# Performance work log

Hardware: AMD Instinct MI355X
Metric: run time of the kernel (lower is better)

Reference implementation:

```python
import jax, jax.numpy as jnp
import numpy as np

N, E = 50000, 800000
NFEAT, HID, NHEAD, NCLASS = 256, 32, 8, 40
NEG_SLOPE = 0.2


def gat_conv(x, src, dst, W, a_src, a_dst, bias, heads, out_ch, concat):
    n = x.shape[0]
    h = (x @ W).reshape(n, heads, out_ch)              # [N, H, C]
    alpha_src = jnp.einsum('nhc,hc->nh', h, a_src)     # [N, H]
    alpha_dst = jnp.einsum('nhc,hc->nh', h, a_dst)
    e = jax.nn.leaky_relu(alpha_src[src] + alpha_dst[dst], NEG_SLOPE)  # [E, H]
    # segment softmax over incoming edges of each dst node
    m = jax.ops.segment_max(e, dst, num_segments=n)
    ex = jnp.exp(e - m[dst])
    s = jax.ops.segment_sum(ex, dst, num_segments=n)
    alpha = ex / (s[dst] + 1e-16)                      # [E, H]
    out = jax.ops.segment_sum(h[src] * alpha[:, :, None], dst, num_segments=n)  # [N, H, C]
    out = out.reshape(n, heads * out_ch) if concat else out.mean(axis=1)
    return out + bias


def setup_inputs() -> dict:
    key = jax.random.key(0)
    ks = jax.random.split(key, 12)
    x = jax.random.normal(ks[0], (N, NFEAT), dtype=jnp.float32)
    edge_index = jax.random.randint(ks[1], (2, E), 0, N, dtype=jnp.int64)
    edge_attr = jax.random.normal(ks[2], (E, 8), dtype=jnp.float32)  # unused by the model
    s1 = 1.0 / np.sqrt(NFEAT)
    s2 = 1.0 / np.sqrt(HID * NHEAD)
    W1 = jax.random.normal(ks[3], (NFEAT, NHEAD * HID), dtype=jnp.float32) * s1
    att_src1 = jax.random.normal(ks[4], (NHEAD, HID), dtype=jnp.float32) * 0.1
    att_dst1 = jax.random.normal(ks[5], (NHEAD, HID), dtype=jnp.float32) * 0.1
    b1 = jnp.zeros((NHEAD * HID,), dtype=jnp.float32)
    W2 = jax.random.normal(ks[6], (NHEAD * HID, NCLASS), dtype=jnp.float32) * s2
    att_src2 = jax.random.normal(ks[7], (1, NCLASS), dtype=jnp.float32) * 0.1
    att_dst2 = jax.random.normal(ks[8], (1, NCLASS), dtype=jnp.float32) * 0.1
    b2 = jnp.zeros((NCLASS,), dtype=jnp.float32)
    return {"x": x, "edge_index": edge_index, "edge_attr": edge_attr,
            "W1": W1, "att_src1": att_src1, "att_dst1": att_dst1, "b1": b1,
            "W2": W2, "att_src2": att_src2, "att_dst2": att_dst2, "b2": b2}


def reference(x, edge_index, edge_attr, W1, att_src1, att_dst1, b1, W2, att_src2, att_dst2, b2):
    # eval mode: dropout is identity. GATConv adds self-loops by default.
    n = x.shape[0]
    loops = jnp.arange(n, dtype=edge_index.dtype)
    src = jnp.concatenate([edge_index[0], loops])
    dst = jnp.concatenate([edge_index[1], loops])
    h = jax.nn.elu(gat_conv(x, src, dst, W1, att_src1, att_dst1, b1, NHEAD, HID, True))
    final = gat_conv(h, src, dst, W2, att_src2, att_dst2, b2, 1, NCLASS, False)
    return final, jax.nn.log_softmax(final, axis=1)
```

## Files before the change

kernel.cpp:

```cpp
#include <hip/hip_runtime.h>
#include <hip/hip_bf16.h>
#include <hip/hip_fp16.h>
#include <math.h>

#define NN 50000
#define EE 800000
#define ET 850000
#define F1 256
#define NHEAD 8
#define HID 32
#define NCLASS 40
#define NEG 0.2f

typedef __attribute__((ext_vector_type(8))) short short8_t;
typedef __attribute__((ext_vector_type(4))) float float4_t;

__device__ __forceinline__ int clampN(int v) {
    return v < 0 ? 0 : (v >= NN ? NN - 1 : v);
}
__device__ __forceinline__ unsigned short f2bf(float f) {
    __hip_bfloat16 h = __float2bfloat16(f);
    return __builtin_bit_cast(unsigned short, h);
}
__device__ __forceinline__ float bf2f(unsigned short u) {
    return __uint_as_float((unsigned)u << 16);
}
__device__ __forceinline__ unsigned short f2h(float f) {
    __half h = __float2half(f);
    return __builtin_bit_cast(unsigned short, h);
}
__device__ __forceinline__ float h2f(unsigned short u) {
    __half h = __builtin_bit_cast(__half, u);
    return __half2float(h);
}
__device__ __forceinline__ float hlo2f(unsigned int u) {
    return h2f((unsigned short)(u & 0xFFFFu));
}
__device__ __forceinline__ float hhi2f(unsigned int u) {
    return h2f((unsigned short)(u >> 16));
}

__global__ __launch_bounds__(256) void hist_kernel(const int* __restrict__ ei, int* __restrict__ deg,
                                                   unsigned int* __restrict__ pack) {
    int t = blockIdx.x * 256 + threadIdx.x;
    if (t >= ET) return;
    int d = (t < EE) ? ei[EE + t] : (t - EE);
    d = clampN(d);
    int r = atomicAdd(&deg[d], 1);
    pack[t] = ((unsigned)d << 15) | (unsigned)r;
}

__global__ __launch_bounds__(256) void scan1_kernel(const int* __restrict__ deg, int* __restrict__ off, int* __restrict__ bsum) {
    __shared__ int lds[256];
    int b = blockIdx.x, tid = threadIdx.x;
    int base = b * 1024 + tid * 4;
    int v0 = (base + 0 < NN) ? deg[base + 0] : 0;
    int v1 = (base + 1 < NN) ? deg[base + 1] : 0;
    int v2 = (base + 2 < NN) ? deg[base + 2] : 0;
    int v3 = (base + 3 < NN) ? deg[base + 3] : 0;
    int s1 = v0 + v1, s2 = s1 + v2, s3 = s2 + v3;
    lds[tid] = s3;
    __syncthreads();
    for (int o = 1; o < 256; o <<= 1) {
        int t = (tid >= o) ? lds[tid - o] : 0;
        __syncthreads();
        if (tid >= o) lds[tid] += t;
        __syncthreads();
    }
    int excl = tid ? lds[tid - 1] : 0;
    if (base + 0 < NN) off[base + 1] = excl + v0;
    if (base + 1 < NN) off[base + 2] = excl + s1;
    if (base + 2 < NN) off[base + 3] = excl + s2;
    if (base + 3 < NN) off[base + 4] = excl + s3;
    if (tid == 255) bsum[b] = lds[255];
}

__global__ __launch_bounds__(256) void scan2_kernel(int* __restrict__ bsum, int nb) {
    __shared__ int lds[256];
    int tid = threadIdx.x;
    lds[tid] = (tid < nb) ? bsum[tid] : 0;
    __syncthreads();
    for (int o = 1; o < 256; o <<= 1) {
        int t = (tid >= o) ? lds[tid - o] : 0;
        __syncthreads();
        if (tid >= o) lds[tid] += t;
        __syncthreads();
    }
    if (tid < nb) bsum[tid] = lds[tid];
}

__global__ __launch_bounds__(256) void scan3_kernel(int* __restrict__ off, const int* __restrict__ bsum) {
    int b = blockIdx.x, tid = threadIdx.x;
    if (b == 0 && tid == 0) off[0] = 0;
    if (b == 0) return;
    int add = bsum[b - 1];
    int base = b * 1024 + tid * 4;
    #pragma unroll
    for (int i = 0; i < 4; ++i) {
        if (base + i < NN) off[base + i + 1] += add;
    }
}

__global__ __launch_bounds__(256) void scatter_kernel(const int* __restrict__ ei, const int* __restrict__ off,
                                                      const unsigned int* __restrict__ pack, int* __restrict__ esrc) {
    int t = blockIdx.x * 256 + threadIdx.x;
    if (t >= ET) return;
    unsigned p = pack[t];
    int d = p >> 15;
    int r = p & 0x7FFF;
    int s = (t < EE) ? ei[t] : (t - EE);
    s = clampN(s);
    esrc[off[d] + r] = s;
}

__global__ __launch_bounds__(256) void prep_kernel(const float* __restrict__ W1,
                                                   const float* __restrict__ as1, const float* __restrict__ ad1,
                                                   unsigned short* __restrict__ Bh, unsigned short* __restrict__ Bl) {
    int n = blockIdx.x;
    int k = threadIdx.x;
    float v;
    if (n < 256) {
        v = W1[(size_t)k * 256 + n];
    } else {
        int j = n - 256;
        int h = j & 7;
        const float* att = (j < 8) ? (as1 + h * 32) : (ad1 + h * 32);
        float s = 0.f;
        #pragma unroll
        for (int c = 0; c < 32; ++c) s += W1[(size_t)k * 256 + h * 32 + c] * att[c];
        v = s;
    }
    unsigned short hi = f2bf(v);
    Bh[n * 256 + k] = hi;
    Bl[n * 256 + k] = f2bf(v - bf2f(hi));
}

#define AKP 40
__global__ __launch_bounds__(256, 2) void gemm1_kernel(const float* __restrict__ x,
                                                       const unsigned short* __restrict__ Bh,
                                                       const unsigned short* __restrict__ Bl,
                                                       unsigned short* __restrict__ h1b,
                                                       float* __restrict__ asrc1, float* __restrict__ adst1) {
    __shared__ __align__(16) unsigned short Ah[128 * AKP];
    __shared__ __align__(16) unsigned short Al[128 * AKP];
    __shared__ __align__(16) unsigned short Bhs[272 * AKP];
    __shared__ __align__(16) unsigned short Bls[272 * AKP];
    int tid = threadIdx.x;
    int wave = tid >> 6, lane = tid & 63;
    int quad = lane >> 4, l16 = lane & 15;
    int row0 = blockIdx.x * 128;

    float4_t acc[2][17];
    #pragma unroll
    for (int i = 0; i < 2; ++i)
        #pragma unroll
        for (int j = 0; j < 17; ++j) acc[i][j] = (float4_t){0.f, 0.f, 0.f, 0.f};

    for (int k0 = 0; k0 < 256; k0 += 32) {
        __syncthreads();
        #pragma unroll
        for (int i = 0; i < 4; ++i) {
            int id = i * 256 + tid;
            int r = id >> 3, kq = id & 7;
            int rr = row0 + r; if (rr >= NN) rr = NN - 1;
            float4 v = *(const float4*)(x + (size_t)rr * 256 + k0 + kq * 4);
            ushort4 hi, lo;
            hi.x = f2bf(v.x); lo.x = f2bf(v.x - bf2f(hi.x));
            hi.y = f2bf(v.y); lo.y = f2bf(v.y - bf2f(hi.y));
            hi.z = f2bf(v.z); lo.z = f2bf(v.z - bf2f(hi.z));
            hi.w = f2bf(v.w); lo.w = f2bf(v.w - bf2f(hi.w));
            *(ushort4*)(Ah + r * AKP + kq * 4) = hi;
            *(ushort4*)(Al + r * AKP + kq * 4) = lo;
        }
        for (int id = tid; id < 272 * 4; id += 256) {
            int r = id >> 2, kq = id & 3;
            *(float4*)(Bhs + r * AKP + kq * 8) = *(const float4*)(Bh + (size_t)r * 256 + k0 + kq * 8);
            *(float4*)(Bls + r * AKP + kq * 8) = *(const float4*)(Bl + (size_t)r * 256 + k0 + kq * 8);
        }
        __syncthreads();
        short8_t ah[2], al[2];
        #pragma unroll
        for (int mt = 0; mt < 2; ++mt) {
            int mrow = wave * 32 + mt * 16 + l16;
            ah[mt] = *(const short8_t*)(Ah + mrow * AKP + quad * 8);
            al[mt] = *(const short8_t*)(Al + mrow * AKP + quad * 8);
        }
        #pragma unroll
        for (int nt = 0; nt < 17; ++nt) {
            int nrow = nt * 16 + l16;
            short8_t bh  = *(const short8_t*)(Bhs + nrow * AKP + quad * 8);
            short8_t blo = *(const short8_t*)(Bls + nrow * AKP + quad * 8);
            #pragma unroll
            for (int mt = 0; mt < 2; ++mt) {
                acc[mt][nt] = __builtin_amdgcn_mfma_f32_16x16x32_bf16(ah[mt], bh,  acc[mt][nt], 0, 0, 0);
                acc[mt][nt] = __builtin_amdgcn_mfma_f32_16x16x32_bf16(ah[mt], blo, acc[mt][nt], 0, 0, 0);
                acc[mt][nt] = __builtin_amdgcn_mfma_f32_16x16x32_bf16(al[mt], bh,  acc[mt][nt], 0, 0, 0);
            }
        }
    }
    #pragma unroll
    for (int mt = 0; mt < 2; ++mt) {
        int rbase = row0 + wave * 32 + mt * 16 + quad * 4;
        #pragma unroll
        for (int r = 0; r < 4; ++r) {
            int row = rbase + r;
            if (row >= NN) continue;
            #pragma unroll
            for (int nt = 0; nt < 16; ++nt)
                h1b[(size_t)row * 256 + nt * 16 + l16] = f2h(acc[mt][nt][r]);
            float v = acc[mt][16][r];
            if (l16 < 8) asrc1[row * 8 + l16] = v;
            else         adst1[row * 8 + (l16 - 8)] = v;
        }
    }
}

#define WST 68
__global__ __launch_bounds__(256) void agg1_kernel(const unsigned short* __restrict__ h1b, const float* __restrict__ asrc,
                                                   const float* __restrict__ adst, const int* __restrict__ esrc,
                                                   const int* __restrict__ off,
                                                   const float* __restrict__ b1, unsigned short* __restrict__ hout) {
    __shared__ __align__(16) float wl[4][8 * WST];
    __shared__ __align__(16) int  snl[4][64];
    int tid = threadIdx.x;
    int wave = tid >> 6;
    int wid = blockIdx.x * 4 + wave;
    if (wid >= NN) return;
    int lane = tid & 63;
    int hp = lane & 7;
    int jp = lane >> 3;
    int hc = lane >> 3;
    int c0 = lane * 4;
    float adh_p = adst[wid * 8 + hp];
    int e0 = off[wid], e1 = off[wid + 1];
    float* wlw = wl[wave];
    int* snw = snl[wave];
    const char* hb = (const char*)h1b;
    unsigned lofs = (unsigned)c0 * 2;

    float m = -INFINITY, s = 0.f;
    float ax = 0.f, ay = 0.f, az = 0.f, aw = 0.f;

    for (int base = e0; base < e1; base += 64) {
        int cnt = e1 - base; if (cnt > 64) cnt = 64;
        int snv = esrc[base + (lane < cnt ? lane : cnt - 1)];
        snw[lane] = snv;
        int nch = (cnt + 7) >> 3;
        float ee[8];
        float wmax = -INFINITY;
        #pragma unroll
        for (int cj = 0; cj < 8; ++cj) {
            if (cj >= nch) { ee[cj] = -INFINITY; continue; }
            int jedge = cj * 8 + jp;
            int sj = __shfl(snv, jedge);
            float a = asrc[sj * 8 + hp];
            float e = a + adh_p;
            e = (e >= 0.f) ? e : NEG * e;
            if (jedge >= cnt) e = -INFINITY;
            ee[cj] = e;
            wmax = fmaxf(wmax, e);
        }
        wmax = fmaxf(wmax, __shfl_xor(wmax, 8));
        wmax = fmaxf(wmax, __shfl_xor(wmax, 16));
        wmax = fmaxf(wmax, __shfl_xor(wmax, 32));
        float mn = fmaxf(m, wmax);
        float t = __expf(m - mn);
        m = mn;
        s *= t;
        float tc = __shfl(t, hc);
        ax *= tc; ay *= tc; az *= tc; aw *= tc;
        #pragma unroll
        for (int cj = 0; cj < 8; ++cj) {
            if (cj >= nch) break;
            float w = __expf(ee[cj] - mn);
            s += w;
            wlw[hp * WST + cj * 8 + jp] = w;
        }
        const float* wrow = wlw + hc * WST;
        for (int j = 0; j < cnt; j += 4) {
            float4 w4 = *(const float4*)(wrow + j);
            int4 sn4 = *(const int4*)(snw + j);
            uint2 u0 = *(const uint2*)(hb + (((unsigned)sn4.x << 9) + lofs));
            uint2 u1 = *(const uint2*)(hb + (((unsigned)sn4.y << 9) + lofs));
            uint2 u2 = *(const uint2*)(hb + (((unsigned)sn4.z << 9) + lofs));
            uint2 u3 = *(const uint2*)(hb + (((unsigned)sn4.w << 9) + lofs));
            ax += w4.x * hlo2f(u0.x);
            ay += w4.x * hhi2f(u0.x);
            az += w4.x * hlo2f(u0.y);
            aw += w4.x * hhi2f(u0.y);
            ax += w4.y * hlo2f(u1.x);
            ay += w4.y * hhi2f(u1.x);
            az += w4.y * hlo2f(u1.y);
            aw += w4.y * hhi2f(u1.y);
            ax += w4.z * hlo2f(u2.x);
            ay += w4.z * hhi2f(u2.x);
            az += w4.z * hlo2f(u2.y);
            aw += w4.z * hhi2f(u2.y);
            ax += w4.w * hlo2f(u3.x);
            ay += w4.w * hhi2f(u3.x);
            az += w4.w * hlo2f(u3.y);
            aw += w4.w * hhi2f(u3.y);
        }
    }
    s += __shfl_xor(s, 8);
    s += __shfl_xor(s, 16);
    s += __shfl_xor(s, 32);
    float sh = __shfl(s, hc);
    float inv = 1.f / (sh + 1e-16f);
    float4 b = *(const float4*)(b1 + c0);
    float vx = ax * inv + b.x, vy = ay * inv + b.y, vz = az * inv + b.z, vw = aw * inv + b.w;
    ushort4 o;
    o.x = f2h((vx > 0.f) ? vx : expm1f(vx));
    o.y = f2h((vy > 0.f) ? vy : expm1f(vy));
    o.z = f2h((vz > 0.f) ? vz : expm1f(vz));
    o.w = f2h((vw > 0.f) ? vw : expm1f(vw));
    *(ushort4*)(hout + (size_t)wid * 256 + c0) = o;
}

#define G2_TM 128
#define G2_KC 32
__global__ __launch_bounds__(256) void gemm2_kernel(const unsigned short* __restrict__ h, const float* __restrict__ W2,
                                                    const float* __restrict__ at_s, const float* __restrict__ at_d,
                                                    unsigned short* __restrict__ h2b, float* __restrict__ as2,
                                                    float* __restrict__ ad2) {
    __shared__ __align__(16) float w2s[256 * 40];
    __shared__ __align__(16) float As[G2_KC][132];
    int tid = threadIdx.x;
    for (int i = tid; i < 256 * 40; i += 256) w2s[i] = W2[i];
    int g  = tid & 7;
    int rg = tid >> 3;
    int row0 = blockIdx.x * G2_TM;
    float acc[4][5] = {};
    float ats[5], atd[5];
    #pragma unroll
    for (int j = 0; j < 5; ++j) { ats[j] = at_s[g + 8 * j]; atd[j] = at_d[g + 8 * j]; }

    for (int k0 = 0; k0 < 256; k0 += G2_KC) {
        __syncthreads();
        #pragma unroll
        for (int i = 0; i < 2; ++i) {
            int id = i * 256 + tid;
            int r  = id >> 2;
            int kq = id & 3;
            int rr = row0 + r; if (rr >= NN) rr = NN - 1;
            uint4 u = *(const uint4*)(h + (size_t)rr * 256 + k0 + kq * 8);
            As[kq * 8 + 0][r] = hlo2f(u.x);
            As[kq * 8 + 1][r] = hhi2f(u.x);
            As[kq * 8 + 2][r] = hlo2f(u.y);
            As[kq * 8 + 3][r] = hhi2f(u.y);
            As[kq * 8 + 4][r] = hlo2f(u.z);
            As[kq * 8 + 5][r] = hhi2f(u.z);
            As[kq * 8 + 6][r] = hlo2f(u.w);
            As[kq * 8 + 7][r] = hhi2f(u.w);
        }
        __syncthreads();
        #pragma unroll 4
        for (int k = 0; k < G2_KC; ++k) {
            float4 a = *(const float4*)(&As[k][rg * 4]);
            float w[5];
            #pragma unroll
            for (int j = 0; j < 5; ++j) w[j] = w2s[(k0 + k) * 40 + g + 8 * j];
            float av[4] = {a.x, a.y, a.z, a.w};
            #pragma unroll
            for (int r = 0; r < 4; ++r)
                #pragma unroll
                for (int j = 0; j < 5; ++j)
                    acc[r][j] += av[r] * w[j];
        }
    }

    #pragma unroll
    for (int r = 0; r < 4; ++r) {
        int row = row0 + rg * 4 + r;
        float ps = 0.f, pd = 0.f;
        #pragma unroll
        for (int j = 0; j < 5; ++j) {
            ps += acc[r][j] * ats[j];
            pd += acc[r][j] * atd[j];
        }
        ps += __shfl_xor(ps, 1); pd += __shfl_xor(pd, 1);
        ps += __shfl_xor(ps, 2); pd += __shfl_xor(pd, 2);
        ps += __shfl_xor(ps, 4); pd += __shfl_xor(pd, 4);
        if (row < NN) {
            #pragma unroll
            for (int j = 0; j < 5; ++j) h2b[(size_t)row * 40 + g + 8 * j] = f2h(acc[r][j]);
            if (g == 0) { as2[row] = ps; ad2[row] = pd; }
        }
    }
}

__global__ __launch_bounds__(256) void agg2_kernel(const unsigned short* __restrict__ h2b, const float* __restrict__ asrc,
                                                   const float* __restrict__ adst, const int* __restrict__ esrc,
                                                   const int* __restrict__ off,
                                                   const float* __restrict__ b2, float* __restrict__ outF,
                                                   float* __restrict__ outL) {
    __shared__ __align__(16) float wl2[4][64];
    __shared__ __align__(16) int  snl2[4][64];
    int tid = threadIdx.x;
    int wave = tid >> 6;
    int wid = blockIdx.x * 4 + wave;
    if (wid >= NN) return;
    int lane = tid & 63;
    int c = lane;
    float adh = adst[wid];
    int e0 = off[wid], e1 = off[wid + 1];
    const char* hb = (const char*)h2b + ((unsigned)(c < NCLASS ? c : 0) << 1);
    float* wlw = wl2[wave];
    int* snw = snl2[wave];

    float m = -INFINITY, s = 0.f, acc = 0.f;

    for (int base = e0; base < e1; base += 64) {
        int cnt = e1 - base; if (cnt > 64) cnt = 64;
        int snv = esrc[base + (lane < cnt ? lane : cnt - 1)];
        snw[lane] = snv;
        float a = asrc[snv];
        float e = a + adh;
        e = (e >= 0.f) ? e : NEG * e;
        if (lane >= cnt) e = -INFINITY;
        float cm = e;
        cm = fmaxf(cm, __shfl_xor(cm, 1));
        cm = fmaxf(cm, __shfl_xor(cm, 2));
        cm = fmaxf(cm, __shfl_xor(cm, 4));
        cm = fmaxf(cm, __shfl_xor(cm, 8));
        cm = fmaxf(cm, __shfl_xor(cm, 16));
        cm = fmaxf(cm, __shfl_xor(cm, 32));
        float mn = fmaxf(m, cm);
        float t = __expf(m - mn);
        float w = __expf(e - mn);
        s = s * t + w;
        m = mn;
        wlw[lane] = w;
        acc *= t;
        for (int j = 0; j < cnt; j += 4) {
            float4 w4 = *(const float4*)(wlw + j);
            int4 sn4 = *(const int4*)(snw + j);
            unsigned short v0 = *(const unsigned short*)(hb + (unsigned)sn4.x * 80);
            unsigned short v1 = *(const unsigned short*)(hb + (unsigned)sn4.y * 80);
            unsigned short v2 = *(const unsigned short*)(hb + (unsigned)sn4.z * 80);
            unsigned short v3 = *(const unsigned short*)(hb + (unsigned)sn4.w * 80);
            acc += w4.x * h2f(v0);
            acc += w4.y * h2f(v1);
            acc += w4.z * h2f(v2);
            acc += w4.w * h2f(v3);
        }
    }
    s += __shfl_xor(s, 1);
    s += __shfl_xor(s, 2);
    s += __shfl_xor(s, 4);
    s += __shfl_xor(s, 8);
    s += __shfl_xor(s, 16);
    s += __shfl_xor(s, 32);
    float inv = 1.f / (s + 1e-16f);
    float fin = (c < NCLASS) ? (acc * inv + b2[c]) : -INFINITY;
    if (c < NCLASS) outF[(size_t)wid * 40 + c] = fin;
    float mx = fin;
    for (int o = 32; o; o >>= 1) mx = fmaxf(mx, __shfl_xor(mx, o));
    float ex = (c < NCLASS) ? __expf(fin - mx) : 0.f;
    float sm = ex;
    for (int o = 32; o; o >>= 1) sm += __shfl_xor(sm, o);
    if (c < NCLASS) outL[(size_t)wid * 40 + c] = fin - mx - __logf(sm);
}

extern "C" void kernel_launch(void* const* d_in, const int* in_sizes, int n_in,
                              void* d_out, int out_size, void* d_ws, size_t ws_size,
                              hipStream_t stream) {
    const float* x   = (const float*)d_in[0];
    const int*   ei  = (const int*)d_in[1];
    const float* W1  = (const float*)d_in[3];
    const float* as1 = (const float*)d_in[4];
    const float* ad1 = (const float*)d_in[5];
    const float* b1  = (const float*)d_in[6];
    const float* W2  = (const float*)d_in[7];
    const float* as2c = (const float*)d_in[8];
    const float* ad2c = (const float*)d_in[9];
    const float* b2  = (const float*)d_in[10];

    float* outF = (float*)d_out;
    float* outL = outF + (size_t)NN * NCLASS;

    char* w = (char*)d_ws;
    auto alloc = [&](size_t bytes) {
        void* p = (void*)w;
        w += (bytes + 255) & ~(size_t)255;
        return p;
    };
    unsigned short* h1b = (unsigned short*)alloc((size_t)NN * 256 * 2);
    unsigned short* hbuf = (unsigned short*)alloc((size_t)NN * 256 * 2);
    unsigned short* h2b = (unsigned short*)alloc((size_t)NN * 40 * 2);
    float* asrc1 = (float*)alloc((size_t)NN * 8 * 4);
    float* adst1 = (float*)alloc((size_t)NN * 8 * 4);
    float* asrc2 = (float*)alloc((size_t)NN * 4);
    float* adst2 = (float*)alloc((size_t)NN * 4);
    int* deg    = (int*)alloc((size_t)NN * 4);
    int* off    = (int*)alloc((size_t)(NN + 1) * 4);
    unsigned int* pack = (unsigned int*)alloc((size_t)ET * 4);
    int* esrc   = (int*)alloc((size_t)ET * 4);
    int* bsum   = (int*)alloc(64 * 4);
    unsigned short* W1th = (unsigned short*)alloc((size_t)272 * 256 * 2);
    unsigned short* W1tl = (unsigned short*)alloc((size_t)272 * 256 * 2);

    const int NB_SCAN = (NN + 1023) / 1024;

    hipMemsetAsync(deg, 0, (size_t)NN * 4, stream);

    hist_kernel<<<(ET + 255) / 256, 256, 0, stream>>>(ei, deg, pack);
    scan1_kernel<<<NB_SCAN, 256, 0, stream>>>(deg, off, bsum);
    scan2_kernel<<<1, 256, 0, stream>>>(bsum, NB_SCAN);
    scan3_kernel<<<NB_SCAN, 256, 0, stream>>>(off, bsum);
    scatter_kernel<<<(ET + 255) / 256, 256, 0, stream>>>(ei, off, pack, esrc);

    prep_kernel<<<272, 256, 0, stream>>>(W1, as1, ad1, W1th, W1tl);
    gemm1_kernel<<<(NN + 127) / 128, 256, 0, stream>>>(x, W1th, W1tl, h1b, asrc1, adst1);
    agg1_kernel<<<(NN + 3) / 4, 256, 0, stream>>>(h1b, asrc1, adst1, esrc, off, b1, hbuf);
    gemm2_kernel<<<(NN + G2_TM - 1) / G2_TM, 256, 0, stream>>>(hbuf, W2, as2c, ad2c, h2b, asrc2, adst2);
    agg2_kernel<<<(NN + 3) / 4, 256, 0, stream>>>(h2b, asrc2, adst2, esrc, off, b2, outF, outL);
}
```

Measured before the change: 341.3 us.

## Use fp16 split GEMM and process two destination nodes per wave in aggregation

The first GEMM now splits only x into hi/lo fp16 parts and keeps W1 as a single fp16 matrix, so each tile issues two MFMAs instead of three and stages half the B data. Both aggregation kernels now handle two destination nodes per wave, interleaving their gather loads with scalar (readfirstlane) row addresses and unrolling by 8 edges. This is meant to raise memory-level parallelism and hide gather latency. The trade-offs are lower precision on W1, extra register pressure, and wasted work when the two nodes have very different degrees.

```diff
diff --git a/kernel.cpp b/kernel.cpp
--- a/kernel.cpp
+++ b/kernel.cpp
@@ -13,17 +13,11 @@
 #define NEG 0.2f
 
 typedef __attribute__((ext_vector_type(8))) short short8_t;
+typedef __attribute__((ext_vector_type(8))) _Float16 half8_t;
 typedef __attribute__((ext_vector_type(4))) float float4_t;
 
 __device__ __forceinline__ int clampN(int v) {
     return v < 0 ? 0 : (v >= NN ? NN - 1 : v);
-}
-__device__ __forceinline__ unsigned short f2bf(float f) {
-    __hip_bfloat16 h = __float2bfloat16(f);
-    return __builtin_bit_cast(unsigned short, h);
-}
-__device__ __forceinline__ float bf2f(unsigned short u) {
-    return __uint_as_float((unsigned)u << 16);
 }
 __device__ __forceinline__ unsigned short f2h(float f) {
     __half h = __float2half(f);
@@ -115,7 +109,7 @@
 
 __global__ __launch_bounds__(256) void prep_kernel(const float* __restrict__ W1,
                                                    const float* __restrict__ as1, const float* __restrict__ ad1,
-                                                   unsigned short* __restrict__ Bh, unsigned short* __restrict__ Bl) {
+                                                   unsigned short* __restrict__ Bt) {
     int n = blockIdx.x;
     int k = threadIdx.x;
     float v;
@@ -130,21 +124,17 @@
         for (int c = 0; c < 32; ++c) s += W1[(size_t)k * 256 + h * 32 + c] * att[c];
         v = s;
     }
-    unsigned short hi = f2bf(v);
-    Bh[n * 256 + k] = hi;
-    Bl[n * 256 + k] = f2bf(v - bf2f(hi));
+    Bt[n * 256 + k] = f2h(v);
 }
 
 #define AKP 40
 __global__ __launch_bounds__(256, 2) void gemm1_kernel(const float* __restrict__ x,
-                                                       const unsigned short* __restrict__ Bh,
-                                                       const unsigned short* __restrict__ Bl,
+                                                       const unsigned short* __restrict__ Bt,
                                                        unsigned short* __restrict__ h1b,
                                                        float* __restrict__ asrc1, float* __restrict__ adst1) {
     __shared__ __align__(16) unsigned short Ah[128 * AKP];
     __shared__ __align__(16) unsigned short Al[128 * AKP];
-    __shared__ __align__(16) unsigned short Bhs[272 * AKP];
-    __shared__ __align__(16) unsigned short Bls[272 * AKP];
+    __shared__ __align__(16) unsigned short Bs[272 * AKP];
     int tid = threadIdx.x;
     int wave = tid >> 6, lane = tid & 63;
     int quad = lane >> 4, l16 = lane & 15;
@@ -165,36 +155,33 @@
             int rr = row0 + r; if (rr >= NN) rr = NN - 1;
             float4 v = *(const float4*)(x + (size_t)rr * 256 + k0 + kq * 4);
             ushort4 hi, lo;
-            hi.x = f2bf(v.x); lo.x = f2bf(v.x - bf2f(hi.x));
-            hi.y = f2bf(v.y); lo.y = f2bf(v.y - bf2f(hi.y));
-            hi.z = f2bf(v.z); lo.z = f2bf(v.z - bf2f(hi.z));
-            hi.w = f2bf(v.w); lo.w = f2bf(v.w - bf2f(hi.w));
+            hi.x = f2h(v.x); lo.x = f2h(v.x - h2f(hi.x));
+            hi.y = f2h(v.y); lo.y = f2h(v.y - h2f(hi.y));
+            hi.z = f2h(v.z); lo.z = f2h(v.z - h2f(hi.z));
+            hi.w = f2h(v.w); lo.w = f2h(v.w - h2f(hi.w));
             *(ushort4*)(Ah + r * AKP + kq * 4) = hi;
             *(ushort4*)(Al + r * AKP + kq * 4) = lo;
         }
         for (int id = tid; id < 272 * 4; id += 256) {
             int r = id >> 2, kq = id & 3;
-            *(float4*)(Bhs + r * AKP + kq * 8) = *(const float4*)(Bh + (size_t)r * 256 + k0 + kq * 8);
-            *(float4*)(Bls + r * AKP + kq * 8) = *(const float4*)(Bl + (size_t)r * 256 + k0 + kq * 8);
+            *(float4*)(Bs + r * AKP + kq * 8) = *(const float4*)(Bt + (size_t)r * 256 + k0 + kq * 8);
         }
         __syncthreads();
-        short8_t ah[2], al[2];
+        half8_t ah[2], al[2];
         #pragma unroll
         for (int mt = 0; mt < 2; ++mt) {
             int mrow = wave * 32 + mt * 16 + l16;
-            ah[mt] = *(const short8_t*)(Ah + mrow * AKP + quad * 8);
-            al[mt] = *(const short8_t*)(Al + mrow * AKP + quad * 8);
+            ah[mt] = *(const half8_t*)(Ah + mrow * AKP + quad * 8);
+            al[mt] = *(const half8_t*)(Al + mrow * AKP + quad * 8);
         }
         #pragma unroll
         for (int nt = 0; nt < 17; ++nt) {
             int nrow = nt * 16 + l16;
-            short8_t bh  = *(const short8_t*)(Bhs + nrow * AKP + quad * 8);
-            short8_t blo = *(const short8_t*)(Bls + nrow * AKP + quad * 8);
+            half8_t bh = *(const half8_t*)(Bs + nrow * AKP + quad * 8);
             #pragma unroll
             for (int mt = 0; mt < 2; ++mt) {
-                acc[mt][nt] = __builtin_amdgcn_mfma_f32_16x16x32_bf16(ah[mt], bh,  acc[mt][nt], 0, 0, 0);
-                acc[mt][nt] = __builtin_amdgcn_mfma_f32_16x16x32_bf16(ah[mt], blo, acc[mt][nt], 0, 0, 0);
-                acc[mt][nt] = __builtin_amdgcn_mfma_f32_16x16x32_bf16(al[mt], bh,  acc[mt][nt], 0, 0, 0);
+                acc[mt][nt] = __builtin_amdgcn_mfma_f32_16x16x32_f16(ah[mt], bh, acc[mt][nt], 0, 0, 0);
+                acc[mt][nt] = __builtin_amdgcn_mfma_f32_16x16x32_f16(al[mt], bh, acc[mt][nt], 0, 0, 0);
             }
         }
     }
@@ -220,101 +207,219 @@
                                                    const float* __restrict__ adst, const int* __restrict__ esrc,
                                                    const int* __restrict__ off,
                                                    const float* __restrict__ b1, unsigned short* __restrict__ hout) {
-    __shared__ __align__(16) float wl[4][8 * WST];
-    __shared__ __align__(16) int  snl[4][64];
+    __shared__ __align__(16) float wl[4][2][8 * WST];
+    __shared__ __align__(16) int  snl[4][2][64];
     int tid = threadIdx.x;
     int wave = tid >> 6;
-    int wid = blockIdx.x * 4 + wave;
-    if (wid >= NN) return;
+    int wid0 = blockIdx.x * 8 + wave * 2;
+    if (wid0 >= NN) return;
+    int wid1 = wid0 + 1;
+    bool has1 = (wid1 < NN);
     int lane = tid & 63;
     int hp = lane & 7;
     int jp = lane >> 3;
     int hc = lane >> 3;
     int c0 = lane * 4;
-    float adh_p = adst[wid * 8 + hp];
-    int e0 = off[wid], e1 = off[wid + 1];
-    float* wlw = wl[wave];
-    int* snw = snl[wave];
+    float* wlw0 = wl[wave][0];
+    float* wlw1 = wl[wave][1];
+    int* snw0 = snl[wave][0];
+    int* snw1 = snl[wave][1];
+    const float* wrow0 = wlw0 + hc * WST;
+    const float* wrow1 = wlw1 + hc * WST;
     const char* hb = (const char*)h1b;
     unsigned lofs = (unsigned)c0 * 2;
-
-    float m = -INFINITY, s = 0.f;
-    float ax = 0.f, ay = 0.f, az = 0.f, aw = 0.f;
-
-    for (int base = e0; base < e1; base += 64) {
-        int cnt = e1 - base; if (cnt > 64) cnt = 64;
-        int snv = esrc[base + (lane < cnt ? lane : cnt - 1)];
-        snw[lane] = snv;
-        int nch = (cnt + 7) >> 3;
-        float ee[8];
-        float wmax = -INFINITY;
-        #pragma unroll
-        for (int cj = 0; cj < 8; ++cj) {
-            if (cj >= nch) { ee[cj] = -INFINITY; continue; }
-            int jedge = cj * 8 + jp;
-            int sj = __shfl(snv, jedge);
-            float a = asrc[sj * 8 + hp];
-            float e = a + adh_p;
-            e = (e >= 0.f) ? e : NEG * e;
-            if (jedge >= cnt) e = -INFINITY;
-            ee[cj] = e;
-            wmax = fmaxf(wmax, e);
-        }
-        wmax = fmaxf(wmax, __shfl_xor(wmax, 8));
-        wmax = fmaxf(wmax, __shfl_xor(wmax, 16));
-        wmax = fmaxf(wmax, __shfl_xor(wmax, 32));
-        float mn = fmaxf(m, wmax);
-        float t = __expf(m - mn);
-        m = mn;
-        s *= t;
-        float tc = __shfl(t, hc);
-        ax *= tc; ay *= tc; az *= tc; aw *= tc;
-        #pragma unroll
-        for (int cj = 0; cj < 8; ++cj) {
-            if (cj >= nch) break;
-            float w = __expf(ee[cj] - mn);
-            s += w;
-            wlw[hp * WST + cj * 8 + jp] = w;
-        }
-        const float* wrow = wlw + hc * WST;
-        for (int j = 0; j < cnt; j += 4) {
-            float4 w4 = *(const float4*)(wrow + j);
-            int4 sn4 = *(const int4*)(snw + j);
-            uint2 u0 = *(const uint2*)(hb + (((unsigned)sn4.x << 9) + lofs));
-            uint2 u1 = *(const uint2*)(hb + (((unsigned)sn4.y << 9) + lofs));
-            uint2 u2 = *(const uint2*)(hb + (((unsigned)sn4.z << 9) + lofs));
-            uint2 u3 = *(const uint2*)(hb + (((unsigned)sn4.w << 9) + lofs));
-            ax += w4.x * hlo2f(u0.x);
-            ay += w4.x * hhi2f(u0.x);
-            az += w4.x * hlo2f(u0.y);
-            aw += w4.x * hhi2f(u0.y);
-            ax += w4.y * hlo2f(u1.x);
-            ay += w4.y * hhi2f(u1.x);
-            az += w4.y * hlo2f(u1.y);
-            aw += w4.y * hhi2f(u1.y);
-            ax += w4.z * hlo2f(u2.x);
-            ay += w4.z * hhi2f(u2.x);
-            az += w4.z * hlo2f(u2.y);
-            aw += w4.z * hhi2f(u2.y);
-            ax += w4.w * hlo2f(u3.x);
-            ay += w4.w * hhi2f(u3.x);
-            az += w4.w * hlo2f(u3.y);
-            aw += w4.w * hhi2f(u3.y);
-        }
-    }
-    s += __shfl_xor(s, 8);
-    s += __shfl_xor(s, 16);
-    s += __shfl_xor(s, 32);
-    float sh = __shfl(s, hc);
-    float inv = 1.f / (sh + 1e-16f);
+    float adh0 = adst[wid0 * 8 + hp];
+    float adh1 = has1 ? adst[wid1 * 8 + hp] : 0.f;
+    int e1_0 = off[wid0 + 1], base0 = off[wid0];
+    int e1_1 = has1 ? off[wid1 + 1] : 0;
+    int base1 = has1 ? off[wid1] : 0;
+
+    float m0 = -INFINITY, s0 = 0.f;
+    float m1 = -INFINITY, s1 = 0.f;
+    float ax0 = 0.f, ay0 = 0.f, az0 = 0.f, aw0 = 0.f;
+    float ax1 = 0.f, ay1 = 0.f, az1 = 0.f, aw1 = 0.f;
+
+    while (base0 < e1_0 || base1 < e1_1) {
+        int cnt0 = e1_0 - base0; cnt0 = cnt0 < 0 ? 0 : (cnt0 > 64 ? 64 : cnt0);
+        int cnt1 = e1_1 - base1; cnt1 = cnt1 < 0 ? 0 : (cnt1 > 64 ? 64 : cnt1);
+        int nch0 = (cnt0 + 7) >> 3;
+        int nch1 = (cnt1 + 7) >> 3;
+        int snv0 = 0, snv1 = 0;
+        if (cnt0 > 0) { snv0 = esrc[base0 + (lane < cnt0 ? lane : cnt0 - 1)]; snw0[lane] = snv0; }
+        if (cnt1 > 0) { snv1 = esrc[base1 + (lane < cnt1 ? lane : cnt1 - 1)]; snw1[lane] = snv1; }
+        float ee0[8], ee1[8];
+        float wmax0 = -INFINITY, wmax1 = -INFINITY;
+        if (cnt0 > 0) {
+            #pragma unroll
+            for (int cj = 0; cj < 8; ++cj) {
+                if (cj >= nch0) { ee0[cj] = -INFINITY; continue; }
+                int jedge = cj * 8 + jp;
+                int sj = __shfl(snv0, jedge);
+                float a = asrc[sj * 8 + hp];
+                float e = a + adh0;
+                e = (e >= 0.f) ? e : NEG * e;
+                if (jedge >= cnt0) e = -INFINITY;
+                ee0[cj] = e;
+                wmax0 = fmaxf(wmax0, e);
+            }
+        }
+        if (cnt1 > 0) {
+            #pragma unroll
+            for (int cj = 0; cj < 8; ++cj) {
+                if (cj >= nch1) { ee1[cj] = -INFINITY; continue; }
+                int jedge = cj * 8 + jp;
+                int sj = __shfl(snv1, jedge);
+                float a = asrc[sj * 8 + hp];
+                float e = a + adh1;
+                e = (e >= 0.f) ? e : NEG * e;
+                if (jedge >= cnt1) e = -INFINITY;
+                ee1[cj] = e;
+                wmax1 = fmaxf(wmax1, e);
+            }
+        }
+        if (cnt0 > 0) {
+            wmax0 = fmaxf(wmax0, __shfl_xor(wmax0, 8));
+            wmax0 = fmaxf(wmax0, __shfl_xor(wmax0, 16));
+            wmax0 = fmaxf(wmax0, __shfl_xor(wmax0, 32));
+            float mn = fmaxf(m0, wmax0);
+            float t = __expf(m0 - mn);
+            m0 = mn;
+            s0 *= t;
+            float tc = __shfl(t, hc);
+            ax0 *= tc; ay0 *= tc; az0 *= tc; aw0 *= tc;
+            #pragma unroll
+            for (int cj = 0; cj < 8; ++cj) {
+                if (cj >= nch0) break;
+                float w = __expf(ee0[cj] - mn);
+                s0 += w;
+                wlw0[hp * WST + cj * 8 + jp] = w;
+            }
+        }
+        if (cnt1 > 0) {
+            wmax1 = fmaxf(wmax1, __shfl_xor(wmax1, 8));
+            wmax1 = fmaxf(wmax1, __shfl_xor(wmax1, 16));
+            wmax1 = fmaxf(wmax1, __shfl_xor(wmax1, 32));
+            float mn = fmaxf(m1, wmax1);
+            float t = __expf(m1 - mn);
+            m1 = mn;
+            s1 *= t;
+            float tc = __shfl(t, hc);
+            ax1 *= tc; ay1 *= tc; az1 *= tc; aw1 *= tc;
+            #pragma unroll
+            for (int cj = 0; cj < 8; ++cj) {
+                if (cj >= nch1) break;
+                float w = __expf(ee1[cj] - mn);
+                s1 += w;
+                wlw1[hp * WST + cj * 8 + jp] = w;
+            }
+        }
+        int nslots0 = (cnt0 > 0) ? nch0 * 8 : 0;
+        int nslots1 = (cnt1 > 0) ? nch1 * 8 : 0;
+        int jmax = nslots0 > nslots1 ? nslots0 : nslots1;
+        for (int j = 0; j < jmax; j += 8) {
+            float4 wa0, wb0, wa1, wb1;
+            uint2 u0, u1, u2, u3, u4, u5, u6, u7;
+            uint2 v0, v1, v2, v3, v4, v5, v6, v7;
+            bool g0 = j < nslots0, g1 = j < nslots1;
+            if (g0) {
+                wa0 = *(const float4*)(wrow0 + j);
+                wb0 = *(const float4*)(wrow0 + j + 4);
+                int4 sa = *(const int4*)(snw0 + j);
+                int4 sb = *(const int4*)(snw0 + j + 4);
+                const char* r0 = hb + ((size_t)(unsigned)__builtin_amdgcn_readfirstlane(sa.x) << 9);
+                const char* r1 = hb + ((size_t)(unsigned)__builtin_amdgcn_readfirstlane(sa.y) << 9);
+                const char* r2 = hb + ((size_t)(unsigned)__builtin_amdgcn_readfirstlane(sa.z) << 9);
+                const char* r3 = hb + ((size_t)(unsigned)__builtin_amdgcn_readfirstlane(sa.w) << 9);
+                const char* r4 = hb + ((size_t)(unsigned)__builtin_amdgcn_readfirstlane(sb.x) << 9);
+                const char* r5 = hb + ((size_t)(unsigned)__builtin_amdgcn_readfirstlane(sb.y) << 9);
+                const char* r6 = hb + ((size_t)(unsigned)__builtin_amdgcn_readfirstlane(sb.z) << 9);
+                const char* r7 = hb + ((size_t)(unsigned)__builtin_amdgcn_readfirstlane(sb.w) << 9);
+                u0 = *(const uint2*)(r0 + lofs);
+                u1 = *(const uint2*)(r1 + lofs);
+                u2 = *(const uint2*)(r2 + lofs);
+                u3 = *(const uint2*)(r3 + lofs);
+                u4 = *(const uint2*)(r4 + lofs);
+                u5 = *(const uint2*)(r5 + lofs);
+                u6 = *(const uint2*)(r6 + lofs);
+                u7 = *(const uint2*)(r7 + lofs);
+            }
+            if (g1) {
+                wa1 = *(const float4*)(wrow1 + j);
+                wb1 = *(const float4*)(wrow1 + j + 4);
+                int4 sa = *(const int4*)(snw1 + j);
+                int4 sb = *(const int4*)(snw1 + j + 4);
+                const char* r0 = hb + ((size_t)(unsigned)__builtin_amdgcn_readfirstlane(sa.x) << 9);
+                const char* r1 = hb + ((size_t)(unsigned)__builtin_amdgcn_readfirstlane(sa.y) << 9);
+                const char* r2 = hb + ((size_t)(unsigned)__builtin_amdgcn_readfirstlane(sa.z) << 9);
+                const char* r3 = hb + ((size_t)(unsigned)__builtin_amdgcn_readfirstlane(sa.w) << 9);
+                const char* r4 = hb + ((size_t)(unsigned)__builtin_amdgcn_readfirstlane(sb.x) << 9);
+                const char* r5 = hb + ((size_t)(unsigned)__builtin_amdgcn_readfirstlane(sb.y) << 9);
+                const char* r6 = hb + ((size_t)(unsigned)__builtin_amdgcn_readfirstlane(sb.z) << 9);
+                const char* r7 = hb + ((size_t)(unsigned)__builtin_amdgcn_readfirstlane(sb.w) << 9);
+                v0 = *(const uint2*)(r0 + lofs);
+                v1 = *(const uint2*)(r1 + lofs);
+                v2 = *(const uint2*)(r2 + lofs);
+                v3 = *(const uint2*)(r3 + lofs);
+                v4 = *(const uint2*)(r4 + lofs);
+                v5 = *(const uint2*)(r5 + lofs);
+                v6 = *(const uint2*)(r6 + lofs);
+                v7 = *(const uint2*)(r7 + lofs);
+            }
+            if (g0) {
+                ax0 += wa0.x * hlo2f(u0.x); ay0 += wa0.x * hhi2f(u0.x); az0 += wa0.x * hlo2f(u0.y); aw0 += wa0.x * hhi2f(u0.y);
+                ax0 += wa0.y * hlo2f(u1.x); ay0 += wa0.y * hhi2f(u1.x); az0 += wa0.y * hlo2f(u1.y); aw0 += wa0.y * hhi2f(u1.y);
+                ax0 += wa0.z * hlo2f(u2.x); ay0 += wa0.z * hhi2f(u2.x); az0 += wa0.z * hlo2f(u2.y); aw0 += wa0.z * hhi2f(u2.y);
+                ax0 += wa0.w * hlo2f(u3.x); ay0 += wa0.w * hhi2f(u3.x); az0 += wa0.w * hlo2f(u3.y); aw0 += wa0.w * hhi2f(u3.y);
+                ax0 += wb0.x * hlo2f(u4.x); ay0 += wb0.x * hhi2f(u4.x); az0 += wb0.x * hlo2f(u4.y); aw0 += wb0.x * hhi2f(u4.y);
+                ax0 += wb0.y * hlo2f(u5.x); ay0 += wb0.y * hhi2f(u5.x); az0 += wb0.y * hlo2f(u5.y); aw0 += wb0.y * hhi2f(u5.y);
+                ax0 += wb0.z * hlo2f(u6.x); ay0 += wb0.z * hhi2f(u6.x); az0 += wb0.z * hlo2f(u6.y); aw0 += wb0.z * hhi2f(u6.y);
+                ax0 += wb0.w * hlo2f(u7.x); ay0 += wb0.w * hhi2f(u7.x); az0 += wb0.w * hlo2f(u7.y); aw0 += wb0.w * hhi2f(u7.y);
+            }
+            if (g1) {
+                ax1 += wa1.x * hlo2f(v0.x); ay1 += wa1.x * hhi2f(v0.x); az1 += wa1.x * hlo2f(v0.y); aw1 += wa1.x * hhi2f(v0.y);
+                ax1 += wa1.y * hlo2f(v1.x); ay1 += wa1.y * hhi2f(v1.x); az1 += wa1.y * hlo2f(v1.y); aw1 += wa1.y * hhi2f(v1.y);
+                ax1 += wa1.z * hlo2f(v2.x); ay1 += wa1.z * hhi2f(v2.x); az1 += wa1.z * hlo2f(v2.y); aw1 += wa1.z * hhi2f(v2.y);
+                ax1 += wa1.w * hlo2f(v3.x); ay1 += wa1.w * hhi2f(v3.x); az1 += wa1.w * hlo2f(v3.y); aw1 += wa1.w * hhi2f(v3.y);
+                ax1 += wb1.x * hlo2f(v4.x); ay1 += wb1.x * hhi2f(v4.x); az1 += wb1.x * hlo2f(v4.y); aw1 += wb1.x * hhi2f(v4.y);
+                ax1 += wb1.y * hlo2f(v5.x); ay1 += wb1.y * hhi2f(v5.x); az1 += wb1.y * hlo2f(v5.y); aw1 += wb1.y * hhi2f(v5.y);
+                ax1 += wb1.z * hlo2f(v6.x); ay1 += wb1.z * hhi2f(v6.x); az1 += wb1.z * hlo2f(v6.y); aw1 += wb1.z * hhi2f(v6.y);
+                ax1 += wb1.w * hlo2f(v7.x); ay1 += wb1.w * hhi2f(v7.x); az1 += wb1.w * hlo2f(v7.y); aw1 += wb1.w * hhi2f(v7.y);
+            }
+        }
+        base0 += 64;
+        base1 += 64;
+    }
     float4 b = *(const float4*)(b1 + c0);
-    float vx = ax * inv + b.x, vy = ay * inv + b.y, vz = az * inv + b.z, vw = aw * inv + b.w;
-    ushort4 o;
-    o.x = f2h((vx > 0.f) ? vx : expm1f(vx));
-    o.y = f2h((vy > 0.f) ? vy : expm1f(vy));
-    o.z = f2h((vz > 0.f) ? vz : expm1f(vz));
-    o.w = f2h((vw > 0.f) ? vw : expm1f(vw));
-    *(ushort4*)(hout + (size_t)wid * 256 + c0) = o;
+    {
+        float s = s0;
+        s += __shfl_xor(s, 8);
+        s += __shfl_xor(s, 16);
+        s += __shfl_xor(s, 32);
+        float sh = __shfl(s, hc);
+        float inv = 1.f / (sh + 1e-16f);
+        float vx = ax0 * inv + b.x, vy = ay0 * inv + b.y, vz = az0 * inv + b.z, vw = aw0 * inv + b.w;
+        ushort4 o;
+        o.x = f2h((vx > 0.f) ? vx : expm1f(vx));
+        o.y = f2h((vy > 0.f) ? vy : expm1f(vy));
+        o.z = f2h((vz > 0.f) ? vz : expm1f(vz));
+        o.w = f2h((vw > 0.f) ? vw : expm1f(vw));
+        *(ushort4*)(hout + (size_t)wid0 * 256 + c0) = o;
+    }
+    {
+        float s = s1;
+        s += __shfl_xor(s, 8);
+        s += __shfl_xor(s, 16);
+        s += __shfl_xor(s, 32);
+        float sh = __shfl(s, hc);
+        float inv = 1.f / (sh + 1e-16f);
+        float vx = ax1 * inv + b.x, vy = ay1 * inv + b.y, vz = az1 * inv + b.z, vw = aw1 * inv + b.w;
+        ushort4 o;
+        o.x = f2h((vx > 0.f) ? vx : expm1f(vx));
+        o.y = f2h((vy > 0.f) ? vy : expm1f(vy));
+        o.z = f2h((vz > 0.f) ? vz : expm1f(vz));
+        o.w = f2h((vw > 0.f) ? vw : expm1f(vw));
+        if (has1) *(ushort4*)(hout + (size_t)wid1 * 256 + c0) = o;
+    }
 }
 
 #define G2_TM 128
@@ -394,72 +499,174 @@
                                                    const int* __restrict__ off,
                                                    const float* __restrict__ b2, float* __restrict__ outF,
                                                    float* __restrict__ outL) {
-    __shared__ __align__(16) float wl2[4][64];
-    __shared__ __align__(16) int  snl2[4][64];
+    __shared__ __align__(16) float wl2[4][2][64];
+    __shared__ __align__(16) int  snl2[4][2][64];
     int tid = threadIdx.x;
     int wave = tid >> 6;
-    int wid = blockIdx.x * 4 + wave;
-    if (wid >= NN) return;
+    int wid0 = blockIdx.x * 8 + wave * 2;
+    if (wid0 >= NN) return;
+    int wid1 = wid0 + 1;
+    bool has1 = (wid1 < NN);
     int lane = tid & 63;
     int c = lane;
-    float adh = adst[wid];
-    int e0 = off[wid], e1 = off[wid + 1];
-    const char* hb = (const char*)h2b + ((unsigned)(c < NCLASS ? c : 0) << 1);
-    float* wlw = wl2[wave];
-    int* snw = snl2[wave];
-
-    float m = -INFINITY, s = 0.f, acc = 0.f;
-
-    for (int base = e0; base < e1; base += 64) {
-        int cnt = e1 - base; if (cnt > 64) cnt = 64;
-        int snv = esrc[base + (lane < cnt ? lane : cnt - 1)];
-        snw[lane] = snv;
-        float a = asrc[snv];
-        float e = a + adh;
-        e = (e >= 0.f) ? e : NEG * e;
-        if (lane >= cnt) e = -INFINITY;
-        float cm = e;
-        cm = fmaxf(cm, __shfl_xor(cm, 1));
-        cm = fmaxf(cm, __shfl_xor(cm, 2));
-        cm = fmaxf(cm, __shfl_xor(cm, 4));
-        cm = fmaxf(cm, __shfl_xor(cm, 8));
-        cm = fmaxf(cm, __shfl_xor(cm, 16));
-        cm = fmaxf(cm, __shfl_xor(cm, 32));
-        float mn = fmaxf(m, cm);
-        float t = __expf(m - mn);
-        float w = __expf(e - mn);
-        s = s * t + w;
-        m = mn;
-        wlw[lane] = w;
-        acc *= t;
-        for (int j = 0; j < cnt; j += 4) {
-            float4 w4 = *(const float4*)(wlw + j);
-            int4 sn4 = *(const int4*)(snw + j);
-            unsigned short v0 = *(const unsigned short*)(hb + (unsigned)sn4.x * 80);
-            unsigned short v1 = *(const unsigned short*)(hb + (unsigned)sn4.y * 80);
-            unsigned short v2 = *(const unsigned short*)(hb + (unsigned)sn4.z * 80);
-            unsigned short v3 = *(const unsigned short*)(hb + (unsigned)sn4.w * 80);
-            acc += w4.x * h2f(v0);
-            acc += w4.y * h2f(v1);
-            acc += w4.z * h2f(v2);
-            acc += w4.w * h2f(v3);
-        }
-    }
-    s += __shfl_xor(s, 1);
-    s += __shfl_xor(s, 2);
-    s += __shfl_xor(s, 4);
-    s += __shfl_xor(s, 8);
-    s += __shfl_xor(s, 16);
-    s += __shfl_xor(s, 32);
-    float inv = 1.f / (s + 1e-16f);
-    float fin = (c < NCLASS) ? (acc * inv + b2[c]) : -INFINITY;
-    if (c < NCLASS) outF[(size_t)wid * 40 + c] = fin;
-    float mx = fin;
-    for (int o = 32; o; o >>= 1) mx = fmaxf(mx, __shfl_xor(mx, o));
-    float ex = (c < NCLASS) ? __expf(fin - mx) : 0.f;
-    float sm = ex;
-    for (int o = 32; o; o >>= 1) sm += __shfl_xor(sm, o);
-    if (c < NCLASS) outL[(size_t)wid * 40 + c] = fin - mx - __logf(sm);
+    const char* hb = (const char*)h2b;
+    unsigned coff = (unsigned)(c < NCLASS ? c : 0) * 2;
+    float* wlw0 = wl2[wave][0];
+    float* wlw1 = wl2[wave][1];
+    int* snw0 = snl2[wave][0];
+    int* snw1 = snl2[wave][1];
+    float bc = (c < NCLASS) ? b2[c] : 0.f;
+    float adh0 = adst[wid0];
+    float adh1 = has1 ? adst[wid1] : 0.f;
+    int e1_0 = off[wid0 + 1], base0 = off[wid0];
+    int e1_1 = has1 ? off[wid1 + 1] : 0;
+    int base1 = has1 ? off[wid1] : 0;
+
+    float m0 = -INFINITY, s0 = 0.f, acc0 = 0.f;
+    float m1 = -INFINITY, s1 = 0.f, acc1 = 0.f;
+
+    while (base0 < e1_0 || base1 < e1_1) {
+        int cnt0 = e1_0 - base0; cnt0 = cnt0 < 0 ? 0 : (cnt0 > 64 ? 64 : cnt0);
+        int cnt1 = e1_1 - base1; cnt1 = cnt1 < 0 ? 0 : (cnt1 > 64 ? 64 : cnt1);
+        int snv0 = 0, snv1 = 0;
+        if (cnt0 > 0) { snv0 = esrc[base0 + (lane < cnt0 ? lane : cnt0 - 1)]; snw0[lane] = snv0; }
+        if (cnt1 > 0) { snv1 = esrc[base1 + (lane < cnt1 ? lane : cnt1 - 1)]; snw1[lane] = snv1; }
+        if (cnt0 > 0) {
+            float a = asrc[snv0];
+            float e = a + adh0;
+            e = (e >= 0.f) ? e : NEG * e;
+            if (lane >= cnt0) e = -INFINITY;
+            float cm = e;
+            cm = fmaxf(cm, __shfl_xor(cm, 1));
+            cm = fmaxf(cm, __shfl_xor(cm, 2));
+            cm = fmaxf(cm, __shfl_xor(cm, 4));
+            cm = fmaxf(cm, __shfl_xor(cm, 8));
+            cm = fmaxf(cm, __shfl_xor(cm, 16));
+            cm = fmaxf(cm, __shfl_xor(cm, 32));
+            float mn = fmaxf(m0, cm);
+            float t = __expf(m0 - mn);
+            float w = __expf(e - mn);
+            s0 = s0 * t + w;
+            m0 = mn;
+            wlw0[lane] = w;
+            acc0 *= t;
+        }
+        if (cnt1 > 0) {
+            float a = asrc[snv1];
+            float e = a + adh1;
+            e = (e >= 0.f) ? e : NEG * e;
+            if (lane >= cnt1) e = -INFINITY;
+            float cm = e;
+            cm = fmaxf(cm, __shfl_xor(cm, 1));
+            cm = fmaxf(cm, __shfl_xor(cm, 2));
+            cm = fmaxf(cm, __shfl_xor(cm, 4));
+            cm = fmaxf(cm, __shfl_xor(cm, 8));
+            cm = fmaxf(cm, __shfl_xor(cm, 16));
+            cm = fmaxf(cm, __shfl_xor(cm, 32));
+            float mn = fmaxf(m1, cm);
+            float t = __expf(m1 - mn);
+            float w = __expf(e - mn);
+            s1 = s1 * t + w;
+            m1 = mn;
+            wlw1[lane] = w;
+            acc1 *= t;
+        }
+        int n8_0 = (cnt0 > 0) ? ((cnt0 + 7) & ~7) : 0;
+        int n8_1 = (cnt1 > 0) ? ((cnt1 + 7) & ~7) : 0;
+        int jmax = n8_0 > n8_1 ? n8_0 : n8_1;
+        for (int j = 0; j < jmax; j += 8) {
+            bool g0 = j < n8_0, g1 = j < n8_1;
+            float4 wa0, wb0, wa1, wb1;
+            unsigned short u0, u1, u2, u3, u4, u5, u6, u7;
+            unsigned short v0, v1, v2, v3, v4, v5, v6, v7;
+            if (g0) {
+                wa0 = *(const float4*)(wlw0 + j);
+                wb0 = *(const float4*)(wlw0 + j + 4);
+                int4 sa = *(const int4*)(snw0 + j);
+                int4 sb = *(const int4*)(snw0 + j + 4);
+                u0 = *(const unsigned short*)(hb + (size_t)((unsigned)__builtin_amdgcn_readfirstlane(sa.x) * 80u) + coff);
+                u1 = *(const unsigned short*)(hb + (size_t)((unsigned)__builtin_amdgcn_readfirstlane(sa.y) * 80u) + coff);
+                u2 = *(const unsigned short*)(hb + (size_t)((unsigned)__builtin_amdgcn_readfirstlane(sa.z) * 80u) + coff);
+                u3 = *(const unsigned short*)(hb + (size_t)((unsigned)__builtin_amdgcn_readfirstlane(sa.w) * 80u) + coff);
+                u4 = *(const unsigned short*)(hb + (size_t)((unsigned)__builtin_amdgcn_readfirstlane(sb.x) * 80u) + coff);
+                u5 = *(const unsigned short*)(hb + (size_t)((unsigned)__builtin_amdgcn_readfirstlane(sb.y) * 80u) + coff);
+                u6 = *(const unsigned short*)(hb + (size_t)((unsigned)__builtin_amdgcn_readfirstlane(sb.z) * 80u) + coff);
+                u7 = *(const unsigned short*)(hb + (size_t)((unsigned)__builtin_amdgcn_readfirstlane(sb.w) * 80u) + coff);
+            }
+            if (g1) {
+                wa1 = *(const float4*)(wlw1 + j);
+                wb1 = *(const float4*)(wlw1 + j + 4);
+                int4 sa = *(const int4*)(snw1 + j);
+                int4 sb = *(const int4*)(snw1 + j + 4);
+                v0 = *(const unsigned short*)(hb + (size_t)((unsigned)__builtin_amdgcn_readfirstlane(sa.x) * 80u) + coff);
+                v1 = *(const unsigned short*)(hb + (size_t)((unsigned)__builtin_amdgcn_readfirstlane(sa.y) * 80u) + coff);
+                v2 = *(const unsigned short*)(hb + (size_t)((unsigned)__builtin_amdgcn_readfirstlane(sa.z) * 80u) + coff);
+                v3 = *(const unsigned short*)(hb + (size_t)((unsigned)__builtin_amdgcn_readfirstlane(sa.w) * 80u) + coff);
+                v4 = *(const unsigned short*)(hb + (size_t)((unsigned)__builtin_amdgcn_readfirstlane(sb.x) * 80u) + coff);
+                v5 = *(const unsigned short*)(hb + (size_t)((unsigned)__builtin_amdgcn_readfirstlane(sb.y) * 80u) + coff);
+                v6 = *(const unsigned short*)(hb + (size_t)((unsigned)__builtin_amdgcn_readfirstlane(sb.z) * 80u) + coff);
+                v7 = *(const unsigned short*)(hb + (size_t)((unsigned)__builtin_amdgcn_readfirstlane(sb.w) * 80u) + coff);
+            }
+            if (g0) {
+                acc0 += wa0.x * h2f(u0);
+                acc0 += wa0.y * h2f(u1);
+                acc0 += wa0.z * h2f(u2);
+                acc0 += wa0.w * h2f(u3);
+                acc0 += wb0.x * h2f(u4);
+                acc0 += wb0.y * h2f(u5);
+                acc0 += wb0.z * h2f(u6);
+                acc0 += wb0.w * h2f(u7);
+            }
+            if (g1) {
+                acc1 += wa1.x * h2f(v0);
+                acc1 += wa1.y * h2f(v1);
+                acc1 += wa1.z * h2f(v2);
+                acc1 += wa1.w * h2f(v3);
+                acc1 += wb1.x * h2f(v4);
+                acc1 += wb1.y * h2f(v5);
+                acc1 += wb1.z * h2f(v6);
+                acc1 += wb1.w * h2f(v7);
+            }
+        }
+        base0 += 64;
+        base1 += 64;
+    }
+    {
+        float s = s0;
+        s += __shfl_xor(s, 1);
+        s += __shfl_xor(s, 2);
+        s += __shfl_xor(s, 4);
+        s += __shfl_xor(s, 8);
+        s += __shfl_xor(s, 16);
+        s += __shfl_xor(s, 32);
+        float inv = 1.f / (s + 1e-16f);
+        float fin = (c < NCLASS) ? (acc0 * inv + bc) : -INFINITY;
+        if (c < NCLASS) outF[(size_t)wid0 * 40 + c] = fin;
+        float mx = fin;
+        for (int o = 32; o; o >>= 1) mx = fmaxf(mx, __shfl_xor(mx, o));
+        float ex = (c < NCLASS) ? __expf(fin - mx) : 0.f;
+        float sm = ex;
+        for (int o = 32; o; o >>= 1) sm += __shfl_xor(sm, o);
+        if (c < NCLASS) outL[(size_t)wid0 * 40 + c] = fin - mx - __logf(sm);
+    }
+    {
+        float s = s1;
+        s += __shfl_xor(s, 1);
+        s += __shfl_xor(s, 2);
+        s += __shfl_xor(s, 4);
+        s += __shfl_xor(s, 8);
+        s += __shfl_xor(s, 16);
+        s += __shfl_xor(s, 32);
+        float inv = 1.f / (s + 1e-16f);
+        float fin = (c < NCLASS) ? (acc1 * inv + bc) : -INFINITY;
+        if (has1 && c < NCLASS) outF[(size_t)wid1 * 40 + c] = fin;
+        float mx = fin;
+        for (int o = 32; o; o >>= 1) mx = fmaxf(mx, __shfl_xor(mx, o));
+        float ex = (c < NCLASS) ? __expf(fin - mx) : 0.f;
+        float sm = ex;
+        for (int o = 32; o; o >>= 1) sm += __shfl_xor(sm, o);
+        if (has1 && c < NCLASS) outL[(size_t)wid1 * 40 + c] = fin - mx - __logf(sm);
+    }
 }
 
 extern "C" void kernel_launch(void* const* d_in, const int* in_sizes, int n_in,
@@ -498,7 +705,6 @@
     int* esrc   = (int*)alloc((size_t)ET * 4);
     int* bsum   = (int*)alloc(64 * 4);
     unsigned short* W1th = (unsigned short*)alloc((size_t)272 * 256 * 2);
-    unsigned short* W1tl = (unsigned short*)alloc((size_t)272 * 256 * 2);
 
     const int NB_SCAN = (NN + 1023) / 1024;
 
@@ -510,9 +716,9 @@
     scan3_kernel<<<NB_SCAN, 256, 0, stream>>>(off, bsum);
     scatter_kernel<<<(ET + 255) / 256, 256, 0, stream>>>(ei, off, pack, esrc);
 
-    prep_kernel<<<272, 256, 0, stream>>>(W1, as1, ad1, W1th, W1tl);
-    gemm1_kernel<<<(NN + 127) / 128, 256, 0, stream>>>(x, W1th, W1tl, h1b, asrc1, adst1);
-    agg1_kernel<<<(NN + 3) / 4, 256, 0, stream>>>(h1b, asrc1, adst1, esrc, off, b1, hbuf);
+    prep_kernel<<<272, 256, 0, stream>>>(W1, as1, ad1, W1th);
+    gemm1_kernel<<<(NN + 127) / 128, 256, 0, stream>>>(x, W1th, h1b, asrc1, adst1);
+    agg1_kernel<<<(NN + 7) / 8, 256, 0, stream>>>(h1b, asrc1, adst1, esrc, off, b1, hbuf);
     gemm2_kernel<<<(NN + G2_TM - 1) / G2_TM, 256, 0, stream>>>(hbuf, W2, as2c, ad2c, h2b, asrc2, adst2);
-    agg2_kernel<<<(NN + 3) / 4, 256, 0, stream>>>(h2b, asrc2, adst2, esrc, off, b2, outF, outL);
-}
+    agg2_kernel<<<(NN + 7) / 8, 256, 0, stream>>>(h2b, asrc2, adst2, esrc, off, b2, outF, outL);
+}
```

New measurement: 342.4 us. No clear change (+0.3%).
